# Kernel optimization log

Measured on AMD Instinct MI355X. Metric: run time of the kernel, lower is better.

The kernel has to match this reference:

```python
import jax, jax.numpy as jnp
import numpy as np

BATCH = 256
VOCAB = 50000
NUM_TOPICS = 50
TIME_SLICES = 10
EMBED_DIM = 1024


def setup_inputs() -> dict:
    key = jax.random.key(0)
    k1, k2, k3, k4 = jax.random.split(key, 4)
    theta = jax.random.uniform(k1, (BATCH, NUM_TOPICS), dtype=jnp.float32)
    theta = theta / jnp.sum(theta, axis=-1, keepdims=True)  # topic distribution
    word_embeddings = jax.random.normal(k2, (VOCAB, EMBED_DIM), dtype=jnp.float32)
    topic_embeddings = jax.random.normal(k3, (TIME_SLICES, NUM_TOPICS, EMBED_DIM), dtype=jnp.float32)
    time_index = jax.random.randint(k4, (BATCH,), 0, TIME_SLICES, dtype=jnp.int64)
    return {"theta": theta, "word_embeddings": word_embeddings,
            "topic_embeddings": topic_embeddings, "time_index": time_index}


def reference(theta, word_embeddings, topic_embeddings, time_index):
    # beta_t = softmax(topic_embeddings[t] @ W^T) over vocab, for all time slices: (T, K, V)
    logits = jnp.einsum('tke,ve->tkv', topic_embeddings, word_embeddings)
    betas = jax.nn.softmax(logits, axis=-1)
    # word_dist[i] = theta[i] @ betas[time_index[i]]. Compute for all t then gather
    # (avoids materializing a (B, K, V) gathered tensor).
    all_out = jnp.einsum('bk,tkv->btv', theta, betas)  # (B, T, V)
    out = jnp.take_along_axis(all_out, time_index[:, None, None], axis=1)[:, 0, :]
    return out  # (B, V)
```

## Files before the change

kernel.cpp:

```cpp
#include <hip/hip_runtime.h>
#include <hip/hip_bf16.h>


typedef __bf16 bf16_t;
typedef __bf16 bf16x4 __attribute__((ext_vector_type(4)));
typedef __bf16 bf16x8 __attribute__((ext_vector_type(8)));
typedef float f32x4 __attribute__((ext_vector_type(4)));

typedef __attribute__((address_space(1))) void gvoid;
typedef __attribute__((address_space(3))) void svoid;
#define GLDS(SRC, DST) \
    __builtin_amdgcn_global_load_lds((gvoid*)(SRC), (svoid*)(DST), 16, 0, 0)
#define MFMA16(A, B, C) __builtin_amdgcn_mfma_f32_16x16x32_bf16((A), (B), (C), 0, 0, 0)

#define SHIFT 180.0f
#define TTS 72

__device__ __forceinline__ void cvt8(float4 a, float4 b, bf16x8& h, bf16x8& l)
{
    float f[8] = {a.x, a.y, a.z, a.w, b.x, b.y, b.z, b.w};
#pragma unroll
    for (int j = 0; j < 8; ++j) {
        bf16_t hh = (bf16_t)f[j];
        h[j] = hh;
        l[j] = (bf16_t)(f[j] - (float)hh);
    }
}

__global__ void prep(const float* __restrict__ x, bf16_t* __restrict__ hi,
                     bf16_t* __restrict__ lo, float* __restrict__ rsum)
{
    int i = blockIdx.x * 256 + threadIdx.x;
    if (i < 512) rsum[i] = 0.f;
    if (i < 512000) {
        float v = x[i];
        bf16_t h = (bf16_t)v;
        hi[i] = h;
        lo[i] = (bf16_t)(v - (float)h);
    }
}

__global__ __launch_bounds__(256, 2)
void gemm_logits(const bf16_t* __restrict__ Ahi, const bf16_t* __restrict__ Alo,
                 const float* __restrict__ W, bf16_t* __restrict__ Pt,
                 float* __restrict__ Rsum)
{
    __shared__ __align__(16) bf16_t sm[32768];
    bf16_t* AsH = sm;
    bf16_t* AsL = sm + 8192;
    bf16_t* BsH = sm + 16384;
    bf16_t* BsL = sm + 24576;

    const int tid = threadIdx.x;
    const int wv = tid >> 6, lane = tid & 63;
    const int bm0 = blockIdx.x * 128;
    const int bn0 = blockIdx.y * 128;
    const int wr = wv >> 1, wc = wv & 1;
    const int lrow = lane & 15, q = lane >> 4;
    const int srow = lane >> 3, sgrp = (lane & 7) ^ srow;

    const int wrow_l = tid >> 1;
    int wrow_g = bn0 + wrow_l; if (wrow_g > 49999) wrow_g = 49999;
    const int half = tid & 1;
    const float* wsrc = W + (long)wrow_g * 1024 + half * 32;

    f32x4 acc[4][4] = {};

    for (int k0 = 0; k0 < 1024; k0 += 64) {
#pragma unroll
        for (int cc = 0; cc < 4; ++cc) {
            const int ch = wv * 4 + cc;
            int ar = bm0 + ch * 8 + srow; if (ar > 499) ar = 499;
            GLDS(Ahi + (long)ar * 1024 + k0 + sgrp * 8, AsH + ch * 512);
            GLDS(Alo + (long)ar * 1024 + k0 + sgrp * 8, AsL + ch * 512);
        }
        {
            const float4* wp = (const float4*)(wsrc + k0);
            float4 f[8];
#pragma unroll
            for (int j = 0; j < 8; ++j) f[j] = wp[j];
#pragma unroll
            for (int j = 0; j < 4; ++j) {
                bf16x8 h, l;
                cvt8(f[2 * j], f[2 * j + 1], h, l);
                const int kg = half * 4 + j;
                const int off = wrow_l * 64 + ((kg ^ (wrow_l & 7)) * 8);
                *(bf16x8*)(BsH + off) = h;
                *(bf16x8*)(BsL + off) = l;
            }
        }
        __syncthreads();
#pragma unroll
        for (int kk = 0; kk < 2; ++kk) {
            const int kg = kk * 4 + q;
            bf16x8 ah[4], al[4], bh[4], bl[4];
#pragma unroll
            for (int a = 0; a < 4; ++a) {
                const int row = wr * 64 + a * 16 + lrow;
                const int off = row * 64 + ((kg ^ (row & 7)) * 8);
                ah[a] = *(const bf16x8*)(AsH + off);
                al[a] = *(const bf16x8*)(AsL + off);
            }
#pragma unroll
            for (int b = 0; b < 4; ++b) {
                const int n = wc * 64 + b * 16 + lrow;
                const int off = n * 64 + ((kg ^ (n & 7)) * 8);
                bh[b] = *(const bf16x8*)(BsH + off);
                bl[b] = *(const bf16x8*)(BsL + off);
            }
#pragma unroll
            for (int a = 0; a < 4; ++a)
#pragma unroll
                for (int b = 0; b < 4; ++b) {
                    acc[a][b] = MFMA16(ah[a], bh[b], acc[a][b]);
                    acc[a][b] = MFMA16(ah[a], bl[b], acc[a][b]);
                    acc[a][b] = MFMA16(al[a], bh[b], acc[a][b]);
                }
        }
        __syncthreads();
    }

    const int colbase = bn0 + wc * 64;
#pragma unroll
    for (int a = 0; a < 4; ++a) {
        float rsum[4] = {0.f, 0.f, 0.f, 0.f};
#pragma unroll
        for (int b = 0; b < 4; ++b) {
            const bool cok = (colbase + b * 16 + lrow) < 50000;
#pragma unroll
            for (int r = 0; r < 4; ++r) {
                const float e = __expf(acc[a][b][r] - SHIFT);
                acc[a][b][r] = e;
                if (cok) rsum[r] += e;
            }
        }
#pragma unroll
        for (int r = 0; r < 4; ++r) {
            float v = rsum[r];
            v += __shfl_xor(v, 1, 16);
            v += __shfl_xor(v, 2, 16);
            v += __shfl_xor(v, 4, 16);
            v += __shfl_xor(v, 8, 16);
            const int row = bm0 + wr * 64 + a * 16 + q * 4 + r;
            if (lrow == 0 && row < 500) atomicAdd(Rsum + row, v);
        }
    }
    bf16_t* Tt = sm + wv * (64 * TTS);
#pragma unroll
    for (int a = 0; a < 4; ++a)
#pragma unroll
        for (int b = 0; b < 4; ++b) {
            bf16x4 p;
#pragma unroll
            for (int r = 0; r < 4; ++r) p[r] = (bf16_t)acc[a][b][r];
            *(bf16x4*)(Tt + (b * 16 + lrow) * TTS + a * 16 + q * 4) = p;
        }
    const long kbase = bm0 + wr * 64;
#pragma unroll
    for (int it = 0; it < 8; ++it) {
        const int u = it * 64 + lane;
        const int vl = u >> 3, ck = u & 7;
        bf16x8 d = *(const bf16x8*)(Tt + vl * TTS + ck * 8);
        *(bf16x8*)(Pt + (long)(colbase + vl) * 512 + kbase + ck * 8) = d;
    }
}

__global__ void build_theta2(const float* __restrict__ theta,
                             const int* __restrict__ tidx,
                             const float* __restrict__ rsum,
                             bf16_t* __restrict__ T2)
{
    const int i = blockIdx.x, r = threadIdx.x;
    const int base = tidx[i] * 50;
    bf16_t v = (bf16_t)0.0f;
    if (r >= base && r < base + 50)
        v = (bf16_t)(theta[i * 50 + (r - base)] / rsum[r]);
    T2[i * 512 + r] = v;
}

__global__ __launch_bounds__(256, 2)
void gemm_out(const bf16_t* __restrict__ T2, const bf16_t* __restrict__ Pt,
              float* __restrict__ out)
{
    __shared__ __align__(16) bf16_t As[256 * 64];
    __shared__ __align__(16) bf16_t Bs[64 * 64];
    const int tid = threadIdx.x;
    const int wave = tid >> 6, lane = tid & 63;
    const int bn0 = blockIdx.x * 64;
    const int lrow = lane & 15, q = lane >> 4;
    const int srow = lane >> 3, sgrp = (lane & 7) ^ srow;

    f32x4 acc[4][4] = {};

    for (int k0 = 0; k0 < 512; k0 += 64) {
#pragma unroll
        for (int cc = 0; cc < 8; ++cc) {
            const int ch = wave * 8 + cc;
            GLDS(T2 + (ch * 8 + srow) * 512 + k0 + sgrp * 8, As + ch * 512);
        }
#pragma unroll
        for (int cc = 0; cc < 2; ++cc) {
            const int ch = wave * 2 + cc;
            const long brow = bn0 + ch * 8 + srow;
            GLDS(Pt + brow * 512 + k0 + sgrp * 8, Bs + ch * 512);
        }
        __syncthreads();
#pragma unroll
        for (int kk = 0; kk < 2; ++kk) {
            const int kg = kk * 4 + q;
            bf16x8 af[4], bfr[4];
#pragma unroll
            for (int a = 0; a < 4; ++a) {
                const int row = wave * 64 + a * 16 + lrow;
                af[a] = *(const bf16x8*)(As + row * 64 + ((kg ^ (row & 7)) * 8));
            }
#pragma unroll
            for (int b = 0; b < 4; ++b) {
                const int n = b * 16 + lrow;
                bfr[b] = *(const bf16x8*)(Bs + n * 64 + ((kg ^ (n & 7)) * 8));
            }
#pragma unroll
            for (int a = 0; a < 4; ++a)
#pragma unroll
                for (int b = 0; b < 4; ++b)
                    acc[a][b] = MFMA16(af[a], bfr[b], acc[a][b]);
        }
        __syncthreads();
    }
#pragma unroll
    for (int a = 0; a < 4; ++a) {
        const int row0 = wave * 64 + a * 16 + q * 4;
#pragma unroll
        for (int b = 0; b < 4; ++b) {
            const int col = bn0 + b * 16 + lrow;
            if (col < 50000) {
#pragma unroll
                for (int r = 0; r < 4; ++r)
                    out[(long)(row0 + r) * 50000 + col] = acc[a][b][r];
            }
        }
    }
}

extern "C" void kernel_launch(void* const* d_in, const int* in_sizes, int n_in,
                              void* d_out, int out_size, void* d_ws, size_t ws_size,
                              hipStream_t stream)
{
    const float* theta = (const float*)d_in[0];
    const float* wemb  = (const float*)d_in[1];
    const float* temb  = (const float*)d_in[2];
    const int*   tidx  = (const int*)d_in[3];
    float* out = (float*)d_out;

    char* ws = (char*)d_ws;
    bf16_t* Pt    = (bf16_t*)ws;
    float*  rsum  = (float*)(ws + 51249152);
    bf16_t* a_hi  = (bf16_t*)(ws + 51251200);
    bf16_t* a_lo  = (bf16_t*)(ws + 52275200);
    bf16_t* T2    = (bf16_t*)(ws + 53299200);

    prep        <<<dim3(2000),   256, 0, stream>>>(temb, a_hi, a_lo, rsum);
    gemm_logits <<<dim3(4, 391), 256, 0, stream>>>(a_hi, a_lo, wemb, Pt, rsum);
    build_theta2<<<dim3(256),    512, 0, stream>>>(theta, tidx, rsum, T2);
    gemm_out    <<<dim3(782),    256, 0, stream>>>(T2, Pt, out);
}
```

Before: 500.3 us.

## Shrink logits GEMM N-tile to 64, prefetch W registers, raise occupancy

```diff
diff --git a/kernel.cpp b/kernel.cpp
--- a/kernel.cpp
+++ b/kernel.cpp
@@ -14,7 +14,7 @@
 #define MFMA16(A, B, C) __builtin_amdgcn_mfma_f32_16x16x32_bf16((A), (B), (C), 0, 0, 0)
 
 #define SHIFT 180.0f
-#define TTS 72
+#define TTS 40
 
 __device__ __forceinline__ void cvt8(float4 a, float4 b, bf16x8& h, bf16x8& l)
 {
@@ -40,31 +40,37 @@
     }
 }
 
-__global__ __launch_bounds__(256, 2)
+__global__ __launch_bounds__(256, 3)
 void gemm_logits(const bf16_t* __restrict__ Ahi, const bf16_t* __restrict__ Alo,
                  const float* __restrict__ W, bf16_t* __restrict__ Pt,
                  float* __restrict__ Rsum)
 {
-    __shared__ __align__(16) bf16_t sm[32768];
+    __shared__ __align__(16) bf16_t sm[24576];
     bf16_t* AsH = sm;
     bf16_t* AsL = sm + 8192;
     bf16_t* BsH = sm + 16384;
-    bf16_t* BsL = sm + 24576;
+    bf16_t* BsL = sm + 20480;
 
     const int tid = threadIdx.x;
     const int wv = tid >> 6, lane = tid & 63;
     const int bm0 = blockIdx.x * 128;
-    const int bn0 = blockIdx.y * 128;
-    const int wr = wv >> 1, wc = wv & 1;
+    const int bn0 = blockIdx.y * 64;
     const int lrow = lane & 15, q = lane >> 4;
     const int srow = lane >> 3, sgrp = (lane & 7) ^ srow;
 
-    const int wrow_l = tid >> 1;
+    const int wrow_l = tid >> 2;
     int wrow_g = bn0 + wrow_l; if (wrow_g > 49999) wrow_g = 49999;
-    const int half = tid & 1;
-    const float* wsrc = W + (long)wrow_g * 1024 + half * 32;
-
-    f32x4 acc[4][4] = {};
+    const int kq = tid & 3;
+    const float4* wp = (const float4*)(W + (long)wrow_g * 1024 + kq * 16);
+    const int kga = kq * 2;
+    const int so_a = wrow_l * 64 + ((kga ^ (wrow_l & 7)) * 8);
+    const int so_b = wrow_l * 64 + (((kga + 1) ^ (wrow_l & 7)) * 8);
+
+    f32x4 acc[2][4] = {};
+
+    float4 wcur[4], wnxt[4];
+#pragma unroll
+    for (int j = 0; j < 4; ++j) wcur[j] = wp[j];
 
     for (int k0 = 0; k0 < 1024; k0 += 64) {
 #pragma unroll
@@ -74,42 +80,41 @@
             GLDS(Ahi + (long)ar * 1024 + k0 + sgrp * 8, AsH + ch * 512);
             GLDS(Alo + (long)ar * 1024 + k0 + sgrp * 8, AsL + ch * 512);
         }
+        if (k0 < 960) {
+            const int o = (k0 + 64) >> 2;
+#pragma unroll
+            for (int j = 0; j < 4; ++j) wnxt[j] = wp[o + j];
+        }
         {
-            const float4* wp = (const float4*)(wsrc + k0);
-            float4 f[8];
-#pragma unroll
-            for (int j = 0; j < 8; ++j) f[j] = wp[j];
-#pragma unroll
-            for (int j = 0; j < 4; ++j) {
-                bf16x8 h, l;
-                cvt8(f[2 * j], f[2 * j + 1], h, l);
-                const int kg = half * 4 + j;
-                const int off = wrow_l * 64 + ((kg ^ (wrow_l & 7)) * 8);
-                *(bf16x8*)(BsH + off) = h;
-                *(bf16x8*)(BsL + off) = l;
-            }
+            bf16x8 h0, l0, h1, l1;
+            cvt8(wcur[0], wcur[1], h0, l0);
+            cvt8(wcur[2], wcur[3], h1, l1);
+            *(bf16x8*)(BsH + so_a) = h0;
+            *(bf16x8*)(BsL + so_a) = l0;
+            *(bf16x8*)(BsH + so_b) = h1;
+            *(bf16x8*)(BsL + so_b) = l1;
         }
         __syncthreads();
 #pragma unroll
         for (int kk = 0; kk < 2; ++kk) {
             const int kg = kk * 4 + q;
-            bf16x8 ah[4], al[4], bh[4], bl[4];
-#pragma unroll
-            for (int a = 0; a < 4; ++a) {
-                const int row = wr * 64 + a * 16 + lrow;
+            bf16x8 ah[2], al[2], bh[4], bl[4];
+#pragma unroll
+            for (int a = 0; a < 2; ++a) {
+                const int row = wv * 32 + a * 16 + lrow;
                 const int off = row * 64 + ((kg ^ (row & 7)) * 8);
                 ah[a] = *(const bf16x8*)(AsH + off);
                 al[a] = *(const bf16x8*)(AsL + off);
             }
 #pragma unroll
             for (int b = 0; b < 4; ++b) {
-                const int n = wc * 64 + b * 16 + lrow;
+                const int n = b * 16 + lrow;
                 const int off = n * 64 + ((kg ^ (n & 7)) * 8);
                 bh[b] = *(const bf16x8*)(BsH + off);
                 bl[b] = *(const bf16x8*)(BsL + off);
             }
 #pragma unroll
-            for (int a = 0; a < 4; ++a)
+            for (int a = 0; a < 2; ++a)
 #pragma unroll
                 for (int b = 0; b < 4; ++b) {
                     acc[a][b] = MFMA16(ah[a], bh[b], acc[a][b]);
@@ -118,36 +123,37 @@
                 }
         }
         __syncthreads();
-    }
-
-    const int colbase = bn0 + wc * 64;
-#pragma unroll
-    for (int a = 0; a < 4; ++a) {
-        float rsum[4] = {0.f, 0.f, 0.f, 0.f};
+#pragma unroll
+        for (int j = 0; j < 4; ++j) wcur[j] = wnxt[j];
+    }
+
+#pragma unroll
+    for (int a = 0; a < 2; ++a) {
+        float rs[4] = {0.f, 0.f, 0.f, 0.f};
 #pragma unroll
         for (int b = 0; b < 4; ++b) {
-            const bool cok = (colbase + b * 16 + lrow) < 50000;
+            const bool cok = (bn0 + b * 16 + lrow) < 50000;
 #pragma unroll
             for (int r = 0; r < 4; ++r) {
                 const float e = __expf(acc[a][b][r] - SHIFT);
                 acc[a][b][r] = e;
-                if (cok) rsum[r] += e;
+                if (cok) rs[r] += e;
             }
         }
 #pragma unroll
         for (int r = 0; r < 4; ++r) {
-            float v = rsum[r];
+            float v = rs[r];
             v += __shfl_xor(v, 1, 16);
             v += __shfl_xor(v, 2, 16);
             v += __shfl_xor(v, 4, 16);
             v += __shfl_xor(v, 8, 16);
-            const int row = bm0 + wr * 64 + a * 16 + q * 4 + r;
+            const int row = bm0 + wv * 32 + a * 16 + q * 4 + r;
             if (lrow == 0 && row < 500) atomicAdd(Rsum + row, v);
         }
     }
     bf16_t* Tt = sm + wv * (64 * TTS);
 #pragma unroll
-    for (int a = 0; a < 4; ++a)
+    for (int a = 0; a < 2; ++a)
 #pragma unroll
         for (int b = 0; b < 4; ++b) {
             bf16x4 p;
@@ -155,13 +161,13 @@
             for (int r = 0; r < 4; ++r) p[r] = (bf16_t)acc[a][b][r];
             *(bf16x4*)(Tt + (b * 16 + lrow) * TTS + a * 16 + q * 4) = p;
         }
-    const long kbase = bm0 + wr * 64;
-#pragma unroll
-    for (int it = 0; it < 8; ++it) {
+    const long kbase = bm0 + wv * 32;
+#pragma unroll
+    for (int it = 0; it < 4; ++it) {
         const int u = it * 64 + lane;
-        const int vl = u >> 3, ck = u & 7;
+        const int vl = u >> 2, ck = u & 3;
         bf16x8 d = *(const bf16x8*)(Tt + vl * TTS + ck * 8);
-        *(bf16x8*)(Pt + (long)(colbase + vl) * 512 + kbase + ck * 8) = d;
+        *(bf16x8*)(Pt + (long)(bn0 + vl) * 512 + kbase + ck * 8) = d;
     }
 }
 
@@ -178,7 +184,7 @@
     T2[i * 512 + r] = v;
 }
 
-__global__ __launch_bounds__(256, 2)
+__global__ __launch_bounds__(256, 4)
 void gemm_out(const bf16_t* __restrict__ T2, const bf16_t* __restrict__ Pt,
               float* __restrict__ out)
 {
@@ -260,7 +266,7 @@
     bf16_t* T2    = (bf16_t*)(ws + 53299200);
 
     prep        <<<dim3(2000),   256, 0, stream>>>(temb, a_hi, a_lo, rsum);
-    gemm_logits <<<dim3(4, 391), 256, 0, stream>>>(a_hi, a_lo, wemb, Pt, rsum);
+    gemm_logits <<<dim3(4, 782), 256, 0, stream>>>(a_hi, a_lo, wemb, Pt, rsum);
     build_theta2<<<dim3(256),    512, 0, stream>>>(theta, tidx, rsum, T2);
     gemm_out    <<<dim3(782),    256, 0, stream>>>(T2, Pt, out);
 }
```

Measured after the change: 461.9 us. 1.08x faster.
